# Kernel optimization log

Hardware: AMD Instinct MI355X
Metric: run time of the kernel (lower is better)

## Reference

```python
import jax, jax.numpy as jnp
import numpy as np

N = 100000
E = 3200000
IN_DIM = 128
HID = 128
OUT_DIM = 2
L = 3
P = 2
PART = IN_DIM // P  # 64, equals HID // P
G = 64  # number of graphs
EPS = 1e-5


def setup_inputs() -> dict:
    key = jax.random.key(0)
    ks = jax.random.split(key, 12)
    x = jax.random.normal(ks[0], (N, IN_DIM), dtype=jnp.float32)
    edge_index = jax.random.randint(ks[1], (2, E), 0, N, dtype=jnp.int64)
    batch = jnp.sort(jax.random.randint(ks[2], (N,), 0, G, dtype=jnp.int64))
    # stacked GCNConv params: all convs are PART->PART (64->64)
    W_conv = jax.random.normal(ks[3], (L, P, PART, PART), dtype=jnp.float32) * 0.1
    b_conv = jax.random.normal(ks[4], (L, P, PART), dtype=jnp.float32) * 0.02
    # batchnorm (eval mode, running stats)
    bn_gamma = jnp.ones((L, HID), dtype=jnp.float32) + 0.1 * jax.random.normal(ks[5], (L, HID))
    bn_beta = 0.1 * jax.random.normal(ks[6], (L, HID), dtype=jnp.float32)
    bn_mean = 0.1 * jax.random.normal(ks[7], (L, HID), dtype=jnp.float32)
    bn_var = jnp.ones((L, HID), dtype=jnp.float32) + 0.1 * jax.random.uniform(ks[8], (L, HID))
    W_fc1 = jax.random.normal(ks[9], (HID * L, HID), dtype=jnp.float32) * 0.05
    b_fc1 = jnp.zeros((HID,), dtype=jnp.float32)
    W_fc2 = jax.random.normal(ks[10], (HID, OUT_DIM), dtype=jnp.float32) * 0.05
    b_fc2 = jnp.zeros((OUT_DIM,), dtype=jnp.float32)
    return dict(x=x, edge_index=edge_index, batch=batch, W_conv=W_conv, b_conv=b_conv,
                bn_gamma=bn_gamma, bn_beta=bn_beta, bn_mean=bn_mean, bn_var=bn_var,
                W_fc1=W_fc1, b_fc1=b_fc1, W_fc2=W_fc2, b_fc2=b_fc2)


def _gcn_norm(edge_index, num_nodes):
    # add self loops, compute symmetric normalization (PyG gcn_norm, edge_weight=1)
    loop = jnp.arange(num_nodes, dtype=edge_index.dtype)
    row = jnp.concatenate([edge_index[0], loop])  # source j
    col = jnp.concatenate([edge_index[1], loop])  # target i
    deg = jax.ops.segment_sum(jnp.ones_like(col, dtype=jnp.float32), col, num_segments=num_nodes)
    dis = jnp.where(deg > 0, jax.lax.rsqrt(jnp.maximum(deg, 1.0)), 0.0)
    norm = dis[row] * dis[col]  # [E+N]
    return row, col, norm


def _gcn_conv(xp, W, b, row, col, norm, num_nodes):
    xw = xp @ W                               # [N, PART] linear first (PyG GCNConv)
    msg = xw[row] * norm[:, None]             # gather + scale
    out = jax.ops.segment_sum(msg, col, num_segments=num_nodes)  # scatter-add
    return out + b


def reference(x, edge_index, batch, W_conv, b_conv, bn_gamma, bn_beta, bn_mean, bn_var,
              W_fc1, b_fc1, W_fc2, b_fc2):
    num_nodes = x.shape[0]
    row, col, norm = _gcn_norm(edge_index, num_nodes)
    layer_outputs = []
    h = x
    for l in range(L):
        parts = jnp.split(h, P, axis=-1)
        outs = [_gcn_conv(parts[p], W_conv[l, p], b_conv[l, p], row, col, norm, num_nodes)
                for p in range(P)]
        h = jnp.concatenate(outs, axis=-1)  # [N, HID]
        # BatchNorm1d in eval mode
        h = (h - bn_mean[l]) * jax.lax.rsqrt(bn_var[l] + EPS) * bn_gamma[l] + bn_beta[l]
        h = jax.nn.relu(h)  # dropout inactive in eval
        layer_outputs.append(h)
    hjk = jnp.concatenate(layer_outputs, axis=-1)  # [N, HID*L]
    # global mean pool per graph
    sums = jax.ops.segment_sum(hjk, batch, num_segments=G)
    cnts = jax.ops.segment_sum(jnp.ones((num_nodes,), dtype=jnp.float32), batch, num_segments=G)
    pooled = sums / jnp.maximum(cnts, 1.0)[:, None]  # [G, HID*L]
    z = jax.nn.relu(pooled @ W_fc1 + b_fc1)
    z = z @ W_fc2 + b_fc2
    return jax.nn.log_softmax(z, axis=-1)
```

## Files before the change

### kernel.cpp

```cpp
#include <hip/hip_runtime.h>
#include <cstdint>
#include <cstddef>

#define FEAT 128
#define NLAYERS 3
#define EPS 1e-5f
#define TILE 8192
#define SBSHIFT 9

typedef unsigned int uint32;
typedef float floatx2 __attribute__((ext_vector_type(2)));

__device__ __forceinline__ uint32 pack_bf16(float a, float b) {
  uint32 ua = __float_as_uint(a);
  uint32 ub = __float_as_uint(b);
  ua += 0x7fffu + ((ua >> 16) & 1u);
  ub += 0x7fffu + ((ub >> 16) & 1u);
  return (ua >> 16) | (ub & 0xffff0000u);
}

__global__ void scan1(const int* __restrict__ in, int* __restrict__ bsum, int n) {
  __shared__ int s[256];
  int t = threadIdx.x;
  int i = blockIdx.x * 256 + t;
  s[t] = (i < n) ? in[i] : 0;
  __syncthreads();
  for (int o = 128; o > 0; o >>= 1) {
    if (t < o) s[t] += s[t + o];
    __syncthreads();
  }
  if (t == 0) bsum[blockIdx.x] = s[0];
}

__global__ void scan2(int* __restrict__ bsum, int nb) {
  __shared__ int s[512];
  int t = threadIdx.x;
  int v = (t < nb) ? bsum[t] : 0;
  s[t] = v;
  __syncthreads();
  for (int o = 1; o < 512; o <<= 1) {
    int add = (t >= o) ? s[t - o] : 0;
    __syncthreads();
    s[t] += add;
    __syncthreads();
  }
  if (t < nb) bsum[t] = s[t] - v;
}

__global__ void gscan3(const int* __restrict__ in, const int* __restrict__ bsum,
                       int* __restrict__ out, int n) {
  __shared__ int s[256];
  int t = threadIdx.x;
  int i = blockIdx.x * 256 + t;
  int v = (i < n) ? in[i] : 0;
  s[t] = v;
  __syncthreads();
  for (int o = 1; o < 256; o <<= 1) {
    int add = (t >= o) ? s[t - o] : 0;
    __syncthreads();
    s[t] += add;
    __syncthreads();
  }
  if (i < n) out[i] = bsum[blockIdx.x] + s[t] - v;
}

__global__ __launch_bounds__(256) void l1count_k(const int* __restrict__ col,
                                                 int* __restrict__ C, int E, int NT,
                                                 int SB) {
  __shared__ int h[256];
  int t = threadIdx.x;
  h[t] = 0;
  __syncthreads();
  int base = blockIdx.x * TILE;
  int end = min(base + TILE, E);
  for (int i = base + t; i < end; i += 256) atomicAdd(&h[col[i] >> SBSHIFT], 1);
  __syncthreads();
  if (t < SB) C[t * NT + blockIdx.x] = h[t];
}

__global__ __launch_bounds__(256) void l1scatter_k(const int* __restrict__ row,
                                                   const int* __restrict__ col,
                                                   const int* __restrict__ Cex,
                                                   uint32* __restrict__ bbuf, int E, int NT,
                                                   int SB) {
  __shared__ int cur[256];
  int t = threadIdx.x;
  if (t < SB) cur[t] = Cex[t * NT + blockIdx.x];
  __syncthreads();
  int base = blockIdx.x * TILE;
  int end = min(base + TILE, E);
  for (int i = base + t; i < end; i += 256) {
    int c = col[i];
    int pos = atomicAdd(&cur[c >> SBSHIFT], 1);
    bbuf[pos] = ((uint32)(c & ((1 << SBSHIFT) - 1)) << 17) | (uint32)row[i];
  }
}

__global__ __launch_bounds__(256) void l2_k(const uint32* __restrict__ bbuf,
                                            const int* __restrict__ Cex,
                                            int* __restrict__ rowstart,
                                            float* __restrict__ dis,
                                            int* __restrict__ csrc,
                                            int N, int E, int NT, int SB) {
  __shared__ int hist[512];
  __shared__ int scanbuf[256];
  const int b = blockIdx.x;
  const int t = threadIdx.x;
  const int n0 = b << SBSHIFT;
  hist[t] = 0;
  hist[t + 256] = 0;
  __syncthreads();
  const int s = Cex[b * NT];
  const int e1 = (b == SB - 1) ? E : Cex[(b + 1) * NT];
  for (int i = s + t; i < e1; i += 256) {
    atomicAdd(&hist[bbuf[i] >> 17], 1);
  }
  __syncthreads();
  int a0 = hist[2 * t];
  int a1 = hist[2 * t + 1];
  int pair = a0 + a1;
  scanbuf[t] = pair;
  __syncthreads();
  for (int o = 1; o < 256; o <<= 1) {
    int add = (t >= o) ? scanbuf[t - o] : 0;
    __syncthreads();
    scanbuf[t] += add;
    __syncthreads();
  }
  int pairExcl = scanbuf[t] - pair;
  int c0 = s + pairExcl;
  int c1 = c0 + a0;
  int n = n0 + 2 * t;
  if (n < N) {
    rowstart[n] = c0;
    dis[n] = rsqrtf((float)(a0 + 1));
  }
  if (n + 1 < N) {
    rowstart[n + 1] = c1;
    dis[n + 1] = rsqrtf((float)(a1 + 1));
  }
  if (b == SB - 1 && t == 0) rowstart[N] = E;
  hist[2 * t] = c0;
  hist[2 * t + 1] = c1;
  __syncthreads();
  for (int i = s + t; i < e1; i += 256) {
    uint32 pk = bbuf[i];
    int pos = atomicAdd(&hist[pk >> 17], 1);
    csrc[pos] = (int)(pk & 0x1FFFFu);
  }
}

__global__ __launch_bounds__(256) void prep_k(const int* __restrict__ batch,
                                              int* __restrict__ gstart,
                                              const float* __restrict__ bconv,
                                              const float* __restrict__ gamma,
                                              const float* __restrict__ beta,
                                              const float* __restrict__ mean,
                                              const float* __restrict__ var,
                                              float* __restrict__ bns,
                                              float* __restrict__ bnt,
                                              int N, int G) {
  int t = threadIdx.x;
  if (blockIdx.x < NLAYERS) {
    if (t < FEAT) {
      int i = blockIdx.x * FEAT + t;
      float s = gamma[i] * rsqrtf(var[i] + EPS);
      bns[i] = s;
      bnt[i] = (bconv[i] - mean[i]) * s + beta[i];
    }
    return;
  }
  int n = (blockIdx.x - NLAYERS) * 256 + t;
  if (n >= N) return;
  int b = batch[n];
  int prev = (n == 0) ? -1 : batch[n - 1];
  for (int g = prev + 1; g <= b; ++g) gstart[g] = n;
  if (n == N - 1) {
    for (int g = b + 1; g <= G; ++g) gstart[g] = N;
  }
}

__global__ __launch_bounds__(256) void xw_k(const void* __restrict__ h, int isBf16,
                                            const float* __restrict__ W,
                                            const float* __restrict__ dis,
                                            uint32* __restrict__ xs8, int N) {
  __shared__ float hT[64 * 68];
  __shared__ float Ws[64 * 64];
  const int t = threadIdx.x;
  const int a = t >> 4;
  const int b = t & 15;
  const int base = blockIdx.x * 64;

  for (int p = 0; p < 2; ++p) {
    {
      const float4* src = (const float4*)(W + p * 4096);
      float4* dst = (float4*)Ws;
#pragma unroll
      for (int r = 0; r < 4; ++r) dst[r * 256 + t] = src[r * 256 + t];
    }
#pragma unroll
    for (int r = 0; r < 4; ++r) {
      int qid = r * 256 + t;
      int n = qid >> 4;
      int q = qid & 15;
      float4 v = make_float4(0.f, 0.f, 0.f, 0.f);
      int node = base + n;
      if (node < N) {
        if (isBf16) {
          uint2 wv = *(const uint2*)((const uint32*)h + (size_t)node * 64 + p * 32 + q * 2);
          v.x = __uint_as_float(wv.x << 16);
          v.y = __uint_as_float(wv.x & 0xffff0000u);
          v.z = __uint_as_float(wv.y << 16);
          v.w = __uint_as_float(wv.y & 0xffff0000u);
        } else {
          v = *(const float4*)((const float*)h + (size_t)node * FEAT + p * 64 + q * 4);
        }
      }
      hT[(q * 4 + 0) * 68 + n] = v.x;
      hT[(q * 4 + 1) * 68 + n] = v.y;
      hT[(q * 4 + 2) * 68 + n] = v.z;
      hT[(q * 4 + 3) * 68 + n] = v.w;
    }
    __syncthreads();

    float acc[4][4];
#pragma unroll
    for (int i = 0; i < 4; ++i)
#pragma unroll
      for (int j = 0; j < 4; ++j) acc[i][j] = 0.f;

#pragma unroll 8
    for (int k = 0; k < 64; ++k) {
      float4 hv = *(const float4*)(hT + k * 68 + a * 4);
      float4 wv = *(const float4*)(Ws + k * 64 + b * 4);
      acc[0][0] += hv.x * wv.x; acc[0][1] += hv.x * wv.y; acc[0][2] += hv.x * wv.z; acc[0][3] += hv.x * wv.w;
      acc[1][0] += hv.y * wv.x; acc[1][1] += hv.y * wv.y; acc[1][2] += hv.y * wv.z; acc[1][3] += hv.y * wv.w;
      acc[2][0] += hv.z * wv.x; acc[2][1] += hv.z * wv.y; acc[2][2] += hv.z * wv.z; acc[2][3] += hv.z * wv.w;
      acc[3][0] += hv.w * wv.x; acc[3][1] += hv.w * wv.y; acc[3][2] += hv.w * wv.z; acc[3][3] += hv.w * wv.w;
    }

#pragma unroll
    for (int i = 0; i < 4; ++i) {
      int node = base + a * 4 + i;
      if (node < N) {
        float d = dis[node];
        int w = __builtin_amdgcn_cvt_pk_fp8_f32(acc[i][0] * d, acc[i][1] * d, 0, false);
        w = __builtin_amdgcn_cvt_pk_fp8_f32(acc[i][2] * d, acc[i][3] * d, w, true);
        xs8[(size_t)node * 32 + p * 16 + b] = (uint32)w;
      }
    }
    __syncthreads();
  }
}

__global__ __launch_bounds__(512) void gather_k(const unsigned short* __restrict__ xs8,
                                                const float* __restrict__ dis,
                                                const int* __restrict__ rowstart,
                                                const int* __restrict__ csrc,
                                                const int* __restrict__ batch,
                                                const float* __restrict__ bns,
                                                const float* __restrict__ bnt,
                                                uint32* __restrict__ hout,
                                                float* __restrict__ sums,
                                                int layer, int N) {
  const int w = threadIdx.x >> 6;
  const int lane = threadIdx.x & 63;
  const int wid = blockIdx.x * 8 + w;
  const bool valid = (wid < N);
  const int f = lane * 2;

  float rx = 0.f, ry = 0.f;
  int g = -1;

  if (valid) {
    int e0 = rowstart[wid];
    int e1 = rowstart[wid + 1];
    float di = dis[wid];

    int selfv = xs8[(uint32)wid * 64u + (uint32)lane];
    floatx2 acc = __builtin_amdgcn_cvt_pk_f32_fp8(selfv, false);

    for (int base = e0; base < e1; base += 64) {
      int cnt = min(64, e1 - base);
      int my = (lane < cnt) ? csrc[base + lane] : 0;
      int j = 0;
      for (; j + 15 < cnt; j += 16) {
        uint32 oo[16];
        int vv[16];
#pragma unroll
        for (int u = 0; u < 16; ++u) oo[u] = (uint32)__shfl(my, j + u) * 64u + (uint32)lane;
#pragma unroll
        for (int u = 0; u < 16; ++u) vv[u] = xs8[oo[u]];
#pragma unroll
        for (int u = 0; u < 16; ++u)
          acc += (floatx2)__builtin_amdgcn_cvt_pk_f32_fp8(vv[u], false);
      }
      for (; j + 3 < cnt; j += 4) {
        uint32 oo[4];
        int vv[4];
#pragma unroll
        for (int u = 0; u < 4; ++u) oo[u] = (uint32)__shfl(my, j + u) * 64u + (uint32)lane;
#pragma unroll
        for (int u = 0; u < 4; ++u) vv[u] = xs8[oo[u]];
#pragma unroll
        for (int u = 0; u < 4; ++u)
          acc += (floatx2)__builtin_amdgcn_cvt_pk_f32_fp8(vv[u], false);
      }
      for (; j < cnt; ++j) {
        uint32 off = (uint32)__shfl(my, j) * 64u + (uint32)lane;
        acc += (floatx2)__builtin_amdgcn_cvt_pk_f32_fp8((int)xs8[off], false);
      }
    }
    float ax = acc[0] * di;
    float ay = acc[1] * di;
    rx = fmaxf(ax * bns[f] + bnt[f], 0.f);
    ry = fmaxf(ay * bns[f + 1] + bnt[f + 1], 0.f);
    if (hout) hout[(uint32)wid * 64u + (uint32)lane] = pack_bf16(rx, ry);
    g = batch[wid];
  }

  __shared__ float ps[8][FEAT];
  __shared__ int gs[8];
  if (lane == 0) gs[w] = g;
  *(float2*)&ps[w][f] = make_float2(rx, ry);
  __syncthreads();
  bool same = (gs[0] >= 0);
#pragma unroll
  for (int i = 1; i < 8; ++i) same = same && (gs[i] == gs[0]);
  if (same) {
    int t = threadIdx.x;
    if (t < FEAT) {
      float s = 0.f;
#pragma unroll
      for (int i = 0; i < 8; ++i) s += ps[i][t];
      atomicAdd(&sums[(size_t)gs[0] * (NLAYERS * FEAT) + layer * FEAT + t], s);
    }
  } else if (valid) {
    float* sp = sums + (size_t)g * (NLAYERS * FEAT) + layer * FEAT + f;
    atomicAdd(sp, rx);
    atomicAdd(sp + 1, ry);
  }
}

__global__ __launch_bounds__(128) void head_k(const float* __restrict__ sums,
                                              const int* __restrict__ gstart,
                                              const float* __restrict__ W1,
                                              const float* __restrict__ b1,
                                              const float* __restrict__ W2,
                                              const float* __restrict__ b2,
                                              float* __restrict__ out) {
  __shared__ float pooled[NLAYERS * FEAT];
  __shared__ float z1[FEAT];
  __shared__ float z2[2];
  int g = blockIdx.x;
  int t = threadIdx.x;
  float cnt = (float)(gstart[g + 1] - gstart[g]);
  float inv = 1.f / fmaxf(cnt, 1.f);
  for (int k = t; k < NLAYERS * FEAT; k += 128) pooled[k] = sums[g * (NLAYERS * FEAT) + k] * inv;
  __syncthreads();
  float acc = b1[t];
  for (int k = 0; k < NLAYERS * FEAT; ++k) acc += pooled[k] * W1[k * FEAT + t];
  z1[t] = fmaxf(acc, 0.f);
  __syncthreads();
  if (t < 2) {
    float a = b2[t];
    for (int j = 0; j < FEAT; ++j) a += z1[j] * W2[j * 2 + t];
    z2[t] = a;
  }
  __syncthreads();
  if (t < 2) {
    float m = fmaxf(z2[0], z2[1]);
    float lse = m + logf(expf(z2[0] - m) + expf(z2[1] - m));
    out[g * 2 + t] = z2[t] - lse;
  }
}


extern "C" void kernel_launch(void* const* d_in, const int* in_sizes, int n_in,
                              void* d_out, int out_size, void* d_ws, size_t ws_size,
                              hipStream_t stream) {
  const float* x    = (const float*)d_in[0];
  const int*   ei   = (const int*)d_in[1];
  const int*   batch= (const int*)d_in[2];
  const float* Wc   = (const float*)d_in[3];
  const float* bc   = (const float*)d_in[4];
  const float* gam  = (const float*)d_in[5];
  const float* bet  = (const float*)d_in[6];
  const float* mu   = (const float*)d_in[7];
  const float* var  = (const float*)d_in[8];
  const float* W1   = (const float*)d_in[9];
  const float* b1   = (const float*)d_in[10];
  const float* W2   = (const float*)d_in[11];
  const float* b2   = (const float*)d_in[12];
  float* out = (float*)d_out;

  const int N = in_sizes[0] / FEAT;
  const int E = in_sizes[1] / 2;
  const int G = out_size / 2;
  const int SB = (N + (1 << SBSHIFT) - 1) >> SBSHIFT;
  const int NT = (E + TILE - 1) / TILE;

  const int* row = ei;
  const int* col = ei + E;

  char* p = (char*)d_ws;
  auto alloc = [&](size_t bytes) -> void* {
    void* q = (void*)p;
    p += (bytes + 255) & ~(size_t)255;
    return q;
  };
  float*  dis      = (float*)alloc((size_t)N * 4);
  int*    rowstart = (int*)alloc((size_t)(N + 1) * 4);
  int*    csrc     = (int*)alloc((size_t)E * 4);
  int*    bsum     = (int*)alloc(1024 * 4);
  int*    gstart   = (int*)alloc(1024 * 4);
  int*    C        = (int*)alloc((size_t)256 * NT * 4);
  float*  bns      = (float*)alloc(NLAYERS * FEAT * 4);
  float*  bnt      = (float*)alloc(NLAYERS * FEAT * 4);
  float*  sums     = (float*)alloc((size_t)G * NLAYERS * FEAT * 4);
  uint32* bufA     = (uint32*)alloc((size_t)N * FEAT);
  uint32* bufB     = (uint32*)alloc((size_t)N * 64 * 4);
  uint32* bbuf     = (uint32*)bufB;

  const int nbN = (N + 255) / 256;
  const int Csz = SB * NT;
  const int nbC = (Csz + 255) / 256;

  hipMemsetAsync(sums, 0, (size_t)G * NLAYERS * FEAT * 4, stream);

  l1count_k<<<NT, 256, 0, stream>>>(col, C, E, NT, SB);
  scan1<<<nbC, 256, 0, stream>>>(C, bsum, Csz);
  scan2<<<1, 512, 0, stream>>>(bsum, nbC);
  gscan3<<<nbC, 256, 0, stream>>>(C, bsum, C, Csz);
  l1scatter_k<<<NT, 256, 0, stream>>>(row, col, C, bbuf, E, NT, SB);
  l2_k<<<SB, 256, 0, stream>>>(bbuf, C, rowstart, dis, csrc, N, E, NT, SB);

  prep_k<<<NLAYERS + nbN, 256, 0, stream>>>(batch, gstart, bc, gam, bet, mu, var,
                                            bns, bnt, N, G);

  const int xwBlocks = (N + 63) / 64;
  const int gaBlocks = (N + 7) / 8;
  const void* hin = (const void*)x;
  int isBf16 = 0;
  for (int l = 0; l < NLAYERS; ++l) {
    xw_k<<<xwBlocks, 256, 0, stream>>>(hin, isBf16, Wc + (size_t)l * 8192, dis, bufA, N);
    uint32* hptr = (l == NLAYERS - 1) ? nullptr : bufB;
    gather_k<<<gaBlocks, 512, 0, stream>>>((const unsigned short*)bufA, dis, rowstart,
                                           csrc, batch, bns + l * FEAT, bnt + l * FEAT,
                                           hptr, sums, l, N);
    hin = (const void*)bufB;
    isBf16 = 1;
  }

  head_k<<<G, 128, 0, stream>>>(sums, gstart, W1, b1, W2, b2, out);
}
```

Baseline: 622.3 us.

## Sort nodes by in-degree within each graph to balance gather wavefronts

Adds a per-graph counting sort that orders nodes by in-degree, capped at 255, and stores the permutation in an order array. The gather kernel maps each wavefront to order[idx] instead of the node id, so wavefronts in the same block handle nodes of similar degree and stay within one graph's pooling segment. The goal is less load imbalance and divergence among the waves of a block. The cost is an extra kernel, one more indirection per wavefront, and a loss of locality in the self-feature and output writes.

Measured after the change: 633.5 us. About the same (+1.8%).

```diff
diff --git a/kernel.cpp b/kernel.cpp
--- a/kernel.cpp
+++ b/kernel.cpp
@@ -177,6 +177,39 @@
   for (int g = prev + 1; g <= b; ++g) gstart[g] = n;
   if (n == N - 1) {
     for (int g = b + 1; g <= G; ++g) gstart[g] = N;
+  }
+}
+
+__global__ __launch_bounds__(256) void sort_k(const int* __restrict__ rowstart,
+                                              const int* __restrict__ gstart,
+                                              int* __restrict__ order, int G) {
+  __shared__ int hist[256];
+  __shared__ int scanbuf[256];
+  int g = blockIdx.x;
+  int t = threadIdx.x;
+  int s0 = gstart[g], s1 = gstart[g + 1];
+  hist[t] = 0;
+  __syncthreads();
+  for (int n = s0 + t; n < s1; n += 256) {
+    int deg = rowstart[n + 1] - rowstart[n];
+    atomicAdd(&hist[min(deg, 255)], 1);
+  }
+  __syncthreads();
+  int v = hist[t];
+  scanbuf[t] = v;
+  __syncthreads();
+  for (int o = 1; o < 256; o <<= 1) {
+    int add = (t >= o) ? scanbuf[t - o] : 0;
+    __syncthreads();
+    scanbuf[t] += add;
+    __syncthreads();
+  }
+  hist[t] = s0 + scanbuf[t] - v;
+  __syncthreads();
+  for (int n = s0 + t; n < s1; n += 256) {
+    int deg = rowstart[n + 1] - rowstart[n];
+    int pos = atomicAdd(&hist[min(deg, 255)], 1);
+    order[pos] = n;
   }
 }
 
@@ -258,6 +291,7 @@
                                                 const int* __restrict__ rowstart,
                                                 const int* __restrict__ csrc,
                                                 const int* __restrict__ batch,
+                                                const int* __restrict__ order,
                                                 const float* __restrict__ bns,
                                                 const float* __restrict__ bnt,
                                                 uint32* __restrict__ hout,
@@ -265,8 +299,9 @@
                                                 int layer, int N) {
   const int w = threadIdx.x >> 6;
   const int lane = threadIdx.x & 63;
-  const int wid = blockIdx.x * 8 + w;
-  const bool valid = (wid < N);
+  const int idx = blockIdx.x * 8 + w;
+  const bool valid = (idx < N);
+  const int wid = valid ? order[idx] : 0;
   const int f = lane * 2;
 
   float rx = 0.f, ry = 0.f;
@@ -412,6 +447,7 @@
   float*  dis      = (float*)alloc((size_t)N * 4);
   int*    rowstart = (int*)alloc((size_t)(N + 1) * 4);
   int*    csrc     = (int*)alloc((size_t)E * 4);
+  int*    order    = (int*)alloc((size_t)N * 4);
   int*    bsum     = (int*)alloc(1024 * 4);
   int*    gstart   = (int*)alloc(1024 * 4);
   int*    C        = (int*)alloc((size_t)256 * NT * 4);
@@ -437,6 +473,7 @@
 
   prep_k<<<NLAYERS + nbN, 256, 0, stream>>>(batch, gstart, bc, gam, bet, mu, var,
                                             bns, bnt, N, G);
+  sort_k<<<G, 256, 0, stream>>>(rowstart, gstart, order, G);
 
   const int xwBlocks = (N + 63) / 64;
   const int gaBlocks = (N + 7) / 8;
@@ -446,8 +483,8 @@
     xw_k<<<xwBlocks, 256, 0, stream>>>(hin, isBf16, Wc + (size_t)l * 8192, dis, bufA, N);
     uint32* hptr = (l == NLAYERS - 1) ? nullptr : bufB;
     gather_k<<<gaBlocks, 512, 0, stream>>>((const unsigned short*)bufA, dis, rowstart,
-                                           csrc, batch, bns + l * FEAT, bnt + l * FEAT,
-                                           hptr, sums, l, N);
+                                           csrc, batch, order, bns + l * FEAT,
+                                           bnt + l * FEAT, hptr, sums, l, N);
     hin = (const void*)bufB;
     isBf16 = 1;
   }
```

## Gather four neighbors per wave with 8-byte loads and cross-quarter reduction

Applied to the files above, without the earlier changes.

The gather kernel now splits each 64-lane wave into four 16-lane groups, each loading a full 128-byte fp8 neighbor row with 8-byte loads, so four edges are processed per wave step instead of one row per step with 2-byte loads. Partial sums from the four groups are combined with xor shuffles, and BN, ReLU, the bf16 store and pooling are done by the first quarter with wider vector stores. This cuts the number of load instructions per edge and makes each lane's accesses wider. In exchange it adds shuffle reductions, idle lanes in the epilogue, and padding waste on tail edges.

New measurement: 609.6 us. 2.0% less time.

```diff
diff --git a/kernel.cpp b/kernel.cpp
--- a/kernel.cpp
+++ b/kernel.cpp
@@ -253,7 +253,7 @@
   }
 }
 
-__global__ __launch_bounds__(512) void gather_k(const unsigned short* __restrict__ xs8,
+__global__ __launch_bounds__(512) void gather_k(const uint2* __restrict__ xs2,
                                                 const float* __restrict__ dis,
                                                 const int* __restrict__ rowstart,
                                                 const int* __restrict__ csrc,
@@ -265,11 +265,14 @@
                                                 int layer, int N) {
   const int w = threadIdx.x >> 6;
   const int lane = threadIdx.x & 63;
+  const int sub = lane >> 4;
+  const int d = lane & 15;
   const int wid = blockIdx.x * 8 + w;
   const bool valid = (wid < N);
-  const int f = lane * 2;
-
-  float rx = 0.f, ry = 0.f;
+
+  float r[8];
+#pragma unroll
+  for (int k = 0; k < 8; ++k) r[k] = 0.f;
   int g = -1;
 
   if (valid) {
@@ -277,52 +280,80 @@
     int e1 = rowstart[wid + 1];
     float di = dis[wid];
 
-    int selfv = xs8[(uint32)wid * 64u + (uint32)lane];
-    floatx2 acc = __builtin_amdgcn_cvt_pk_f32_fp8(selfv, false);
+    floatx2 a01 = {0.f, 0.f}, a23 = {0.f, 0.f}, a45 = {0.f, 0.f}, a67 = {0.f, 0.f};
+    {
+      uint2 v = make_uint2(0u, 0u);
+      if (sub == 0) v = xs2[(uint32)wid * 16u + (uint32)d];
+      a01 += (floatx2)__builtin_amdgcn_cvt_pk_f32_fp8((int)v.x, false);
+      a23 += (floatx2)__builtin_amdgcn_cvt_pk_f32_fp8((int)v.x, true);
+      a45 += (floatx2)__builtin_amdgcn_cvt_pk_f32_fp8((int)v.y, false);
+      a67 += (floatx2)__builtin_amdgcn_cvt_pk_f32_fp8((int)v.y, true);
+    }
 
     for (int base = e0; base < e1; base += 64) {
       int cnt = min(64, e1 - base);
       int my = (lane < cnt) ? csrc[base + lane] : 0;
       int j = 0;
       for (; j + 15 < cnt; j += 16) {
-        uint32 oo[16];
-        int vv[16];
-#pragma unroll
-        for (int u = 0; u < 16; ++u) oo[u] = (uint32)__shfl(my, j + u) * 64u + (uint32)lane;
-#pragma unroll
-        for (int u = 0; u < 16; ++u) vv[u] = xs8[oo[u]];
-#pragma unroll
-        for (int u = 0; u < 16; ++u)
-          acc += (floatx2)__builtin_amdgcn_cvt_pk_f32_fp8(vv[u], false);
+        uint2 vv[4];
+#pragma unroll
+        for (int u = 0; u < 4; ++u) {
+          int s = __shfl(my, j + u * 4 + sub);
+          vv[u] = xs2[(uint32)s * 16u + (uint32)d];
+        }
+#pragma unroll
+        for (int u = 0; u < 4; ++u) {
+          a01 += (floatx2)__builtin_amdgcn_cvt_pk_f32_fp8((int)vv[u].x, false);
+          a23 += (floatx2)__builtin_amdgcn_cvt_pk_f32_fp8((int)vv[u].x, true);
+          a45 += (floatx2)__builtin_amdgcn_cvt_pk_f32_fp8((int)vv[u].y, false);
+          a67 += (floatx2)__builtin_amdgcn_cvt_pk_f32_fp8((int)vv[u].y, true);
+        }
       }
-      for (; j + 3 < cnt; j += 4) {
-        uint32 oo[4];
-        int vv[4];
-#pragma unroll
-        for (int u = 0; u < 4; ++u) oo[u] = (uint32)__shfl(my, j + u) * 64u + (uint32)lane;
-#pragma unroll
-        for (int u = 0; u < 4; ++u) vv[u] = xs8[oo[u]];
-#pragma unroll
-        for (int u = 0; u < 4; ++u)
-          acc += (floatx2)__builtin_amdgcn_cvt_pk_f32_fp8(vv[u], false);
+      for (; j < cnt; j += 4) {
+        int ei = j + sub;
+        uint2 v = make_uint2(0u, 0u);
+        if (ei < cnt) {
+          int s = __shfl(my, ei & 63);
+          v = xs2[(uint32)s * 16u + (uint32)d];
+        }
+        a01 += (floatx2)__builtin_amdgcn_cvt_pk_f32_fp8((int)v.x, false);
+        a23 += (floatx2)__builtin_amdgcn_cvt_pk_f32_fp8((int)v.x, true);
+        a45 += (floatx2)__builtin_amdgcn_cvt_pk_f32_fp8((int)v.y, false);
+        a67 += (floatx2)__builtin_amdgcn_cvt_pk_f32_fp8((int)v.y, true);
       }
-      for (; j < cnt; ++j) {
-        uint32 off = (uint32)__shfl(my, j) * 64u + (uint32)lane;
-        acc += (floatx2)__builtin_amdgcn_cvt_pk_f32_fp8((int)xs8[off], false);
-      }
-    }
-    float ax = acc[0] * di;
-    float ay = acc[1] * di;
-    rx = fmaxf(ax * bns[f] + bnt[f], 0.f);
-    ry = fmaxf(ay * bns[f + 1] + bnt[f + 1], 0.f);
-    if (hout) hout[(uint32)wid * 64u + (uint32)lane] = pack_bf16(rx, ry);
+    }
+
+    float acc[8] = {a01[0], a01[1], a23[0], a23[1], a45[0], a45[1], a67[0], a67[1]};
+#pragma unroll
+    for (int k = 0; k < 8; ++k) {
+      acc[k] += __shfl_xor(acc[k], 16);
+      acc[k] += __shfl_xor(acc[k], 32);
+    }
+
+    int fb = 8 * d;
+#pragma unroll
+    for (int k = 0; k < 8; ++k) {
+      float a = acc[k] * di;
+      r[k] = fmaxf(a * bns[fb + k] + bnt[fb + k], 0.f);
+    }
+    if (hout && sub == 0) {
+      uint4 o;
+      o.x = pack_bf16(r[0], r[1]);
+      o.y = pack_bf16(r[2], r[3]);
+      o.z = pack_bf16(r[4], r[5]);
+      o.w = pack_bf16(r[6], r[7]);
+      *(uint4*)(hout + (uint32)wid * 64u + (uint32)d * 4u) = o;
+    }
     g = batch[wid];
   }
 
   __shared__ float ps[8][FEAT];
   __shared__ int gs[8];
   if (lane == 0) gs[w] = g;
-  *(float2*)&ps[w][f] = make_float2(rx, ry);
+  if (sub == 0) {
+    *(float4*)&ps[w][8 * d] = make_float4(r[0], r[1], r[2], r[3]);
+    *(float4*)&ps[w][8 * d + 4] = make_float4(r[4], r[5], r[6], r[7]);
+  }
   __syncthreads();
   bool same = (gs[0] >= 0);
 #pragma unroll
@@ -335,10 +366,10 @@
       for (int i = 0; i < 8; ++i) s += ps[i][t];
       atomicAdd(&sums[(size_t)gs[0] * (NLAYERS * FEAT) + layer * FEAT + t], s);
     }
-  } else if (valid) {
-    float* sp = sums + (size_t)g * (NLAYERS * FEAT) + layer * FEAT + f;
-    atomicAdd(sp, rx);
-    atomicAdd(sp + 1, ry);
+  } else if (valid && sub == 0) {
+    float* sp = sums + (size_t)g * (NLAYERS * FEAT) + layer * FEAT + 8 * d;
+#pragma unroll
+    for (int k = 0; k < 8; ++k) atomicAdd(sp + k, r[k]);
   }
 }
 
@@ -445,7 +476,7 @@
   for (int l = 0; l < NLAYERS; ++l) {
     xw_k<<<xwBlocks, 256, 0, stream>>>(hin, isBf16, Wc + (size_t)l * 8192, dis, bufA, N);
     uint32* hptr = (l == NLAYERS - 1) ? nullptr : bufB;
-    gather_k<<<gaBlocks, 512, 0, stream>>>((const unsigned short*)bufA, dis, rowstart,
+    gather_k<<<gaBlocks, 512, 0, stream>>>((const uint2*)bufA, dis, rowstart,
                                            csrc, batch, bns + l * FEAT, bnt + l * FEAT,
                                            hptr, sums, l, N);
     hin = (const void*)bufB;
```
